# Kernel optimization log

Measured on AMD Instinct MI355X. Metric: run time of the kernel, lower is better.

Reference implementation:

```python
import jax, jax.numpy as jnp
import numpy as np

N = 10000        # nodes
E = 320000       # edges (avg degree 32)
W = 256          # width (assert width >= 256)
H = 8            # num_head (RESCALE_EDGE assumed (1,1) -> nhead=8, dhead=32)
D = W // H       # per-head dim
BOND = 33        # EMBED_BOND[0]
BAG = 3          # indices per edge bag
EPS_GN = 1e-5


def setup_inputs() -> dict:
    key = jax.random.key(0)
    ks = jax.random.split(key, 12)
    x = jax.random.normal(ks[0], (N, W), dtype=jnp.float32)
    edge_idx = jax.random.randint(ks[1], (2, E), 0, N)
    edge_attr = jax.random.randint(ks[2], (E, BAG), 0, BOND)
    # node in-degree wrt scatter target edge_idx[1], clamped to >= 1
    deg = jax.ops.segment_sum(jnp.ones((E,), jnp.float32), edge_idx[1], num_segments=N)
    deg = jnp.maximum(deg, 1.0)
    s = 1.0 / np.sqrt(W)
    W_src = jax.random.normal(ks[3], (W, W), dtype=jnp.float32) * s
    W_tgt = jax.random.normal(ks[4], (W, W), dtype=jnp.float32) * s
    emb = jax.random.normal(ks[5], (BOND, W), dtype=jnp.float32) * 0.02
    emb = emb.at[0].set(0.0)  # padding_idx=0 row is zeros
    sd = 1.0 / np.sqrt(D)
    W_gate = jax.random.normal(ks[6], (H, D, D), dtype=jnp.float32) * sd  # grouped conv1d k=1
    W_val = jax.random.normal(ks[7], (H, D, D), dtype=jnp.float32) * sd
    W_post = jax.random.normal(ks[8], (W, W), dtype=jnp.float32) * s
    deg_param = jnp.zeros((W,), jnp.float32) - 0.01  # DegreeLayer degree_init
    return {"x": x, "deg": deg, "edge_idx": edge_idx, "edge_attr": edge_attr,
            "W_src": W_src, "W_tgt": W_tgt, "emb": emb,
            "W_gate": W_gate, "W_val": W_val, "W_post": W_post,
            "deg_param": deg_param}


def reference(x, deg, edge_idx, edge_attr, W_src, W_tgt, emb, W_gate, W_val, W_post, deg_param):
    # src/tgt 1x1 Conv1d == per-node linear, then edge gather
    xs = x @ W_src.T                      # [N, W]
    xt = x @ W_tgt.T                      # [N, W]
    xx = xs[edge_idx[0]] + xt[edge_idx[1]]  # [E, W]

    # EmbeddingBag(mode='mean', padding_idx=0): padded entries excluded
    mask = (edge_attr != 0).astype(xx.dtype)            # [E, BAG]
    bag = jnp.einsum('ebc,eb->ec', emb[edge_attr], mask)  # [E, W]
    cnt = jnp.maximum(mask.sum(-1, keepdims=True), 1.0)
    gate_bias = bag / cnt

    # GroupNorm(H, W, affine=False) over [E, W, 1]
    xg = xx.reshape(-1, H, D)
    mu = xg.mean(-1, keepdims=True)
    var = xg.var(-1, keepdims=True)
    xn = (xg - mu) / jnp.sqrt(var + EPS_GN)              # [E, H, D]

    # gated grouped 1x1 convs (dropout is identity at eval)
    gin = xn + gate_bias.reshape(-1, H, D)
    gate = jax.nn.relu(jnp.einsum('ehd,hfd->ehf', gin, W_gate))
    val = jnp.einsum('ehd,hfd->ehf', xn, W_val)
    act = (gate * val).reshape(-1, W)                    # [E, W]
    out_e = act @ W_post.T                               # [E, W]

    # scatter-sum to nodes, then degree rescale
    agg = jax.ops.segment_sum(out_e, edge_idx[1], num_segments=x.shape[0])
    return jnp.power(deg[:, None], deg_param) * agg      # [N, W]
```

## Files before the change

### kernel.cpp

```cpp
#include <hip/hip_runtime.h>

#define WID 256
#define EPS_GN 1e-5f

typedef __bf16 v8bf __attribute__((ext_vector_type(8)));
typedef float  v4f  __attribute__((ext_vector_type(4)));

__device__ inline unsigned short f2b(float f) {
    unsigned int u = __builtin_bit_cast(unsigned int, f);
    unsigned int r = (u + 0x7fffu + ((u >> 16) & 1u)) >> 16;
    return (unsigned short)r;
}
__device__ inline __bf16 f2bf(float f) {
    unsigned short s = f2b(f);
    return __builtin_bit_cast(__bf16, s);
}
__device__ inline float lo16(unsigned int u) { return __builtin_bit_cast(float, u << 16); }
__device__ inline float hi16(unsigned int u) { return __builtin_bit_cast(float, u & 0xffff0000u); }

__device__ inline v8bf ld_w8(const float* __restrict__ p) {
    float4 a = *(const float4*)p, b = *(const float4*)(p + 4);
    v8bf r;
    r[0] = f2bf(a.x); r[1] = f2bf(a.y); r[2] = f2bf(a.z); r[3] = f2bf(a.w);
    r[4] = f2bf(b.x); r[5] = f2bf(b.y); r[6] = f2bf(b.z); r[7] = f2bf(b.w);
    return r;
}

__global__ __launch_bounds__(256, 2)
void prepproj_k(const float* __restrict__ x, const float* __restrict__ Wsrc,
                const float* __restrict__ Wtgt, const float* __restrict__ Wp,
                const float* __restrict__ Wg, const float* __restrict__ Wv,
                const float* __restrict__ emb, const int* __restrict__ eidx,
                unsigned short* __restrict__ xsb, unsigned short* __restrict__ xtb,
                unsigned short* __restrict__ Wpb, unsigned short* __restrict__ Wgb,
                unsigned short* __restrict__ Wvb, unsigned short* __restrict__ embWgT,
                int* __restrict__ cnt, float* __restrict__ aggact,
                int N, int E, int BOND, int PB, int AUX) {
    __shared__ unsigned short ab[32 * 264];
    int t = threadIdx.x, b = blockIdx.x;

    if (b >= PB) {
        int atid = (b - PB) * 256 + t, asz = AUX * 256;
        for (int i = atid; i < 65536; i += asz) Wpb[i] = f2b(Wp[i]);
        for (int i = atid; i < 8192; i += asz) { Wgb[i] = f2b(Wg[i]); Wvb[i] = f2b(Wv[i]); }
        for (int i = atid; i < 16384; i += asz) {
            int j = i >> 6, k = i & 63;
            float sacc = 0.f;
            if (k < BOND) {
                int h = j >> 5, f = j & 31;
                const float* er = emb + (size_t)k * WID + h * 32;
                const float* wr = Wg + h * 1024 + f * 32;
#pragma unroll
                for (int d = 0; d < 32; d++) sacc += er[d] * wr[d];
            }
            embWgT[j * 64 + k] = f2b(sacc);
        }
        {
            float4* ap = (float4*)aggact;
            int n4 = (N * WID) >> 2;
            for (int i = atid; i < n4; i += asz) ap[i] = make_float4(0.f, 0.f, 0.f, 0.f);
        }
        for (int i = atid; i < E; i += asz) atomicAdd(&cnt[eidx[E + i]], 1);
        return;
    }

    int n0 = b * 32;
#pragma unroll
    for (int ch = 0; ch < 8; ch++) {
        int flat = ch * 1024 + t * 4;
        int row = flat >> 8, col = flat & 255;
        int n = n0 + row;
        float4 v = (n < N) ? *(const float4*)&x[(size_t)n * WID + col]
                           : make_float4(0.f, 0.f, 0.f, 0.f);
        unsigned int p0 = (unsigned int)f2b(v.x) | ((unsigned int)f2b(v.y) << 16);
        unsigned int p1 = (unsigned int)f2b(v.z) | ((unsigned int)f2b(v.w) << 16);
        *(uint2*)&ab[row * 264 + col] = make_uint2(p0, p1);
    }
    __syncthreads();
    int w = t >> 6, lane = t & 63, m = lane & 15, kg = lane >> 4;
#pragma unroll
    for (int pass = 0; pass < 2; pass++) {
        const float* Wf = pass ? Wtgt : Wsrc;
        unsigned short* outp = pass ? xtb : xsb;
        v4f acc[2][4];
#pragma unroll
        for (int mt = 0; mt < 2; mt++)
#pragma unroll
            for (int nt = 0; nt < 4; nt++) acc[mt][nt] = (v4f){0.f, 0.f, 0.f, 0.f};
#pragma unroll
        for (int kt = 0; kt < 8; kt++) {
            int k0 = kt * 32 + kg * 8;
            v8bf a0 = *(const v8bf*)&ab[m * 264 + k0];
            v8bf a1 = *(const v8bf*)&ab[(16 + m) * 264 + k0];
#pragma unroll
            for (int nt = 0; nt < 4; nt++) {
                int j = w * 64 + nt * 16 + m;
                v8bf bfr = ld_w8(&Wf[j * 256 + k0]);
                acc[0][nt] = __builtin_amdgcn_mfma_f32_16x16x32_bf16(a0, bfr, acc[0][nt], 0, 0, 0);
                acc[1][nt] = __builtin_amdgcn_mfma_f32_16x16x32_bf16(a1, bfr, acc[1][nt], 0, 0, 0);
            }
        }
#pragma unroll
        for (int mt = 0; mt < 2; mt++)
#pragma unroll
            for (int r = 0; r < 4; r++) {
                int n = n0 + mt * 16 + kg * 4 + r;
                if (n < N)
#pragma unroll
                    for (int nt = 0; nt < 4; nt++)
                        outp[(size_t)n * WID + w * 64 + nt * 16 + m] = f2b(acc[mt][nt][r]);
            }
    }
}

__global__ void scan_k(const int* __restrict__ cnt, int* __restrict__ cur, int N) {
    __shared__ int part[1024];
    int t = threadIdx.x;
    int C = (N + 1023) / 1024;
    int s = 0;
    for (int i = 0; i < C; i++) { int idx = t * C + i; if (idx < N) s += cnt[idx]; }
    part[t] = s;
    __syncthreads();
    for (int d = 1; d < 1024; d <<= 1) {
        int v = (t >= d) ? part[t - d] : 0;
        __syncthreads();
        part[t] += v;
        __syncthreads();
    }
    int base = (t == 0) ? 0 : part[t - 1];
    for (int i = 0; i < C; i++) {
        int idx = t * C + i;
        if (idx < N) { cur[idx] = base; base += cnt[idx]; }
    }
}

__global__ void scat_k(const int* __restrict__ eidx, int* __restrict__ cur,
                       int* __restrict__ perm, int E) {
    int i = blockIdx.x * 256 + threadIdx.x;
    if (i < E) { int p = atomicAdd(&cur[eidx[E + i]], 1); perm[p] = i; }
}

__global__ __launch_bounds__(256, 7)
void edge_k(const unsigned short* __restrict__ xsb, const unsigned short* __restrict__ xtb,
            const int* __restrict__ eidx, const int* __restrict__ eattr,
            const int* __restrict__ perm, const unsigned short* __restrict__ Wgb,
            const unsigned short* __restrict__ Wvb, const unsigned short* __restrict__ embWgT,
            float* __restrict__ aggact, int E) {
    __shared__ unsigned short xxb[8704];
    __shared__ unsigned short Mld[32 * 72];
    __shared__ int src_s[32], tgt_s[32];
    __shared__ int segmask_s;

    int t = threadIdx.x;
    int e0 = blockIdx.x * 32;
    int ne = min(32, E - e0);

    {
        int tgtv = -1;
        if (t < 32) {
            int p = (t < ne) ? perm[e0 + t] : -1;
            src_s[t] = (p >= 0) ? eidx[p] : 0;
            tgtv = (p >= 0) ? eidx[E + p] : -1;
            tgt_s[t] = (tgtv >= 0) ? tgtv : 0;
            int a0 = 0, a1 = 0, a2 = 0;
            if (p >= 0) {
                const int* ap = eattr + (size_t)p * 3;
                a0 = ap[0]; a1 = ap[1]; a2 = ap[2];
            }
            unsigned int* Mr = (unsigned int*)&Mld[t * 72];
#pragma unroll
            for (int q = 0; q < 32; q++) Mr[q] = 0;
            int c = (a0 != 0) + (a1 != 0) + (a2 != 0);
            float inv = (p >= 0 && c > 0) ? 1.f / (float)c : 0.f;
            float wa = inv * (float)(1 + (a1 == a0) + (a2 == a0));
            float wb = inv * (float)(1 + (a2 == a1));
            Mld[t * 72 + a0] = f2b(wa);
            if (a1 != a0) Mld[t * 72 + a1] = f2b(wb);
            if (a2 != a0 && a2 != a1) Mld[t * 72 + a2] = f2b(inv);
        }
        if (t < 64) {
            int nxt = __shfl_down(tgtv, 1);
            bool flag = (t < ne) && ((t == ne - 1) || (nxt != tgtv));
            unsigned long long bal = __ballot(flag);
            if (t == 0) segmask_s = (int)(unsigned int)bal;
        }
    }
    __syncthreads();

    {
        int e = t >> 3, c = t & 7;
        int sn = src_s[e], g = tgt_s[e];
        bool live = (e < ne);
        const uint4* ps = (const uint4*)(xsb + (size_t)sn * WID);
        const uint4* pt = (const uint4*)(xtb + (size_t)g * WID);
        uint4 us[4], ut[4];
#pragma unroll
        for (int i = 0; i < 4; i++) { us[i] = ps[c + 8 * i]; ut[i] = pt[c + 8 * i]; }
        float v[4][8], sum[4], sq[4];
#pragma unroll
        for (int i = 0; i < 4; i++) {
            const unsigned int* au = (const unsigned int*)&us[i];
            const unsigned int* bu = (const unsigned int*)&ut[i];
            sum[i] = 0.f; sq[i] = 0.f;
#pragma unroll
            for (int q = 0; q < 4; q++) {
                float x0 = lo16(au[q]) + lo16(bu[q]);
                float x1 = hi16(au[q]) + hi16(bu[q]);
                if (!live) { x0 = 0.f; x1 = 0.f; }
                v[i][2 * q] = x0; v[i][2 * q + 1] = x1;
                sum[i] += x0 + x1;
                sq[i] += x0 * x0 + x1 * x1;
            }
        }
#pragma unroll
        for (int mask = 1; mask <= 2; mask <<= 1)
#pragma unroll
            for (int i = 0; i < 4; i++) {
                sum[i] += __shfl_xor(sum[i], mask);
                sq[i]  += __shfl_xor(sq[i], mask);
            }
#pragma unroll
        for (int i = 0; i < 4; i++) {
            float mu = sum[i] * (1.f / 32.f);
            float var = sq[i] * (1.f / 32.f) - mu * mu;
            float rs = rsqrtf(var + EPS_GN);
            unsigned int pk[4];
#pragma unroll
            for (int q = 0; q < 4; q++) {
                unsigned int l = f2b((v[i][2 * q] - mu) * rs);
                unsigned int h = f2b((v[i][2 * q + 1] - mu) * rs);
                pk[q] = l | (h << 16);
            }
            *(uint4*)&xxb[e * 264 + (c + 8 * i) * 8] = make_uint4(pk[0], pk[1], pk[2], pk[3]);
        }
    }
    __syncthreads();

    {
        int w = t >> 6, lane = t & 63, m = lane & 15, kg = lane >> 4;
        v8bf axn[2][2], aM[2][2];
#pragma unroll
        for (int mt = 0; mt < 2; mt++) {
            int row = mt * 16 + m;
            axn[0][mt] = *(const v8bf*)&xxb[row * 264 + (w * 2 + 0) * 32 + kg * 8];
            axn[1][mt] = *(const v8bf*)&xxb[row * 264 + (w * 2 + 1) * 32 + kg * 8];
            aM[mt][0] = *(const v8bf*)&Mld[row * 72 + kg * 8];
            aM[mt][1] = *(const v8bf*)&Mld[row * 72 + 32 + kg * 8];
        }
        __syncthreads();
        v4f z = {0.f, 0.f, 0.f, 0.f};
#pragma unroll
        for (int hh = 0; hh < 2; hh++) {
            int h = w * 2 + hh;
#pragma unroll
            for (int nt = 0; nt < 2; nt++) {
                int fj = nt * 16 + m;
                int j = h * 32 + fj;
                v8bf bWg = *(const v8bf*)&Wgb[h * 1024 + fj * 32 + kg * 8];
                v8bf bWv = *(const v8bf*)&Wvb[h * 1024 + fj * 32 + kg * 8];
                v8bf bE0 = *(const v8bf*)&embWgT[j * 64 + kg * 8];
                v8bf bE1 = *(const v8bf*)&embWgT[j * 64 + 32 + kg * 8];
#pragma unroll
                for (int mt = 0; mt < 2; mt++) {
                    v4f cgm = __builtin_amdgcn_mfma_f32_16x16x32_bf16(axn[hh][mt], bWg, z, 0, 0, 0);
                    cgm = __builtin_amdgcn_mfma_f32_16x16x32_bf16(aM[mt][0], bE0, cgm, 0, 0, 0);
                    cgm = __builtin_amdgcn_mfma_f32_16x16x32_bf16(aM[mt][1], bE1, cgm, 0, 0, 0);
                    v4f cv = __builtin_amdgcn_mfma_f32_16x16x32_bf16(axn[hh][mt], bWv, z, 0, 0, 0);
#pragma unroll
                    for (int r = 0; r < 4; r++) {
                        int e = mt * 16 + kg * 4 + r;
                        xxb[j * 34 + e] = f2b(fmaxf(cgm[r], 0.f) * cv[r]);
                    }
                }
            }
        }
    }
    __syncthreads();

    {
        unsigned int mask = (unsigned int)__builtin_amdgcn_readfirstlane(segmask_s);
        float sum = 0.f;
#pragma unroll
        for (int i = 0; i < 16; i++) {
            unsigned int r = *(const unsigned int*)&xxb[t * 34 + 2 * i];
            sum += lo16(r);
            if ((mask >> (2 * i)) & 1) {
                int tg = __builtin_amdgcn_readfirstlane(tgt_s[2 * i]);
                atomicAdd(&aggact[(size_t)tg * WID + t], sum);
                sum = 0.f;
            }
            sum += hi16(r);
            if ((mask >> (2 * i + 1)) & 1) {
                int tg = __builtin_amdgcn_readfirstlane(tgt_s[2 * i + 1]);
                atomicAdd(&aggact[(size_t)tg * WID + t], sum);
                sum = 0.f;
            }
        }
    }
}

__global__ __launch_bounds__(256, 2)
void post_k(const float* __restrict__ aggact, const unsigned short* __restrict__ Wpb,
            const float* __restrict__ deg, const float* __restrict__ dp,
            float* __restrict__ out, int N) {
    __shared__ unsigned short ab[32 * 264];
    __shared__ float degl[32];
    int t = threadIdx.x;
    int n0 = blockIdx.x * 32;
#pragma unroll
    for (int ch = 0; ch < 8; ch++) {
        int flat = ch * 1024 + t * 4;
        int row = flat >> 8, col = flat & 255;
        int n = n0 + row;
        float4 v = (n < N) ? *(const float4*)&aggact[(size_t)n * WID + col]
                           : make_float4(0.f, 0.f, 0.f, 0.f);
        unsigned int p0 = (unsigned int)f2b(v.x) | ((unsigned int)f2b(v.y) << 16);
        unsigned int p1 = (unsigned int)f2b(v.z) | ((unsigned int)f2b(v.w) << 16);
        *(uint2*)&ab[row * 264 + col] = make_uint2(p0, p1);
    }
    if (t < 32) {
        int n = n0 + t;
        degl[t] = (n < N) ? log2f(deg[n]) : 0.f;
    }
    __syncthreads();
    int w = t >> 6, lane = t & 63, m = lane & 15, kg = lane >> 4;
    v4f acc[2][4];
#pragma unroll
    for (int mt = 0; mt < 2; mt++)
#pragma unroll
        for (int nt = 0; nt < 4; nt++) acc[mt][nt] = (v4f){0.f, 0.f, 0.f, 0.f};
#pragma unroll
    for (int kt = 0; kt < 8; kt++) {
        int k0 = kt * 32 + kg * 8;
        v8bf a0 = *(const v8bf*)&ab[m * 264 + k0];
        v8bf a1 = *(const v8bf*)&ab[(16 + m) * 264 + k0];
#pragma unroll
        for (int nt = 0; nt < 4; nt++) {
            int j = w * 64 + nt * 16 + m;
            v8bf b = *(const v8bf*)&Wpb[j * 256 + k0];
            acc[0][nt] = __builtin_amdgcn_mfma_f32_16x16x32_bf16(a0, b, acc[0][nt], 0, 0, 0);
            acc[1][nt] = __builtin_amdgcn_mfma_f32_16x16x32_bf16(a1, b, acc[1][nt], 0, 0, 0);
        }
    }
    float dpv[4];
#pragma unroll
    for (int nt = 0; nt < 4; nt++) dpv[nt] = dp[w * 64 + nt * 16 + m];
#pragma unroll
    for (int mt = 0; mt < 2; mt++)
#pragma unroll
        for (int r = 0; r < 4; r++) {
            int row = mt * 16 + kg * 4 + r;
            int n = n0 + row;
            if (n < N) {
                float ld = degl[row];
#pragma unroll
                for (int nt = 0; nt < 4; nt++)
                    out[(size_t)n * WID + w * 64 + nt * 16 + m] =
                        exp2f(dpv[nt] * ld) * acc[mt][nt][r];
            }
        }
}

extern "C" void kernel_launch(void* const* d_in, const int* in_sizes, int n_in,
                              void* d_out, int out_size, void* d_ws, size_t ws_size,
                              hipStream_t stream) {
    const float* x    = (const float*)d_in[0];
    const float* deg  = (const float*)d_in[1];
    const int*   eidx = (const int*)d_in[2];
    const int*   eatt = (const int*)d_in[3];
    const float* Wsrc = (const float*)d_in[4];
    const float* Wtgt = (const float*)d_in[5];
    const float* emb  = (const float*)d_in[6];
    const float* Wg   = (const float*)d_in[7];
    const float* Wv   = (const float*)d_in[8];
    const float* Wp   = (const float*)d_in[9];
    const float* dp   = (const float*)d_in[10];
    int N = in_sizes[0] / WID;
    int E = in_sizes[2] / 2;
    int BOND = in_sizes[6] / WID;

    float* ws     = (float*)d_ws;
    float* aggact = ws;
    int*   cnt    = (int*)(aggact + (size_t)N * WID);
    int*   cur    = cnt + N;
    int*   perm   = cur + N;
    unsigned short* xsb = (unsigned short*)(perm + E);
    unsigned short* xtb = xsb + (size_t)N * WID;
    unsigned short* Wpb = xtb + (size_t)N * WID;
    unsigned short* Wgb = Wpb + 65536;
    unsigned short* Wvb = Wgb + 8192;
    unsigned short* embWgT = Wvb + 8192;

    int PB = (N + 31) / 32;
    int AUX = 128;

    hipMemsetAsync(cnt, 0, (size_t)N * sizeof(int), stream);
    prepproj_k<<<PB + AUX, 256, 0, stream>>>(x, Wsrc, Wtgt, Wp, Wg, Wv, emb, eidx,
                                             xsb, xtb, Wpb, Wgb, Wvb, embWgT, cnt, aggact,
                                             N, E, BOND, PB, AUX);
    scan_k<<<1, 1024, 0, stream>>>(cnt, cur, N);
    scat_k<<<(E + 255) / 256, 256, 0, stream>>>(eidx, cur, perm, E);
    edge_k<<<(E + 31) / 32, 256, 0, stream>>>(xsb, xtb, eidx, eatt, perm, Wgb, Wvb, embWgT, aggact, E);
    post_k<<<(N + 31) / 32, 256, 0, stream>>>(aggact, Wpb, deg, dp, (float*)d_out, N);
}
```

Measured before the change: 237.4 us.

## Use packed bf16 conversion, fdot2 pair sums, and XCD-aware edge tile mapping

Replaces the scalar round-to-nearest bf16 conversions with the hardware packed cvt_pk_bf16_f32 builtin where it is available. It folds the GroupNorm normalize into a single fma and packs the gated activations as 32-bit LDS stores. It also uses fdot2 with a ones vector to add bf16 pairs in the segmented reduction. Finally, it remaps edge block indices so that each of the 8 XCDs gets a contiguous range of sorted edge tiles, which should improve L2 locality for the atomics on target rows, though the grid may now contain a few idle blocks.

```diff
diff --git a/kernel.cpp b/kernel.cpp
--- a/kernel.cpp
+++ b/kernel.cpp
@@ -4,6 +4,7 @@
 #define EPS_GN 1e-5f
 
 typedef __bf16 v8bf __attribute__((ext_vector_type(8)));
+typedef __bf16 v2bf __attribute__((ext_vector_type(2)));
 typedef float  v4f  __attribute__((ext_vector_type(4)));
 
 __device__ inline unsigned short f2b(float f) {
@@ -18,12 +19,35 @@
 __device__ inline float lo16(unsigned int u) { return __builtin_bit_cast(float, u << 16); }
 __device__ inline float hi16(unsigned int u) { return __builtin_bit_cast(float, u & 0xffff0000u); }
 
+#if __has_builtin(__builtin_amdgcn_cvt_pk_bf16_f32)
+__device__ inline unsigned int pkbf(float a, float b) {
+    v2bf r = __builtin_amdgcn_cvt_pk_bf16_f32(a, b);
+    return __builtin_bit_cast(unsigned int, r);
+}
+#else
+__device__ inline unsigned int pkbf(float a, float b) {
+    return (unsigned int)f2b(a) | ((unsigned int)f2b(b) << 16);
+}
+#endif
+
+#if __has_builtin(__builtin_amdgcn_fdot2_f32_bf16)
+__device__ inline float pairsum(unsigned int u, float s) {
+    v2bf p = __builtin_bit_cast(v2bf, u);
+    v2bf ones = __builtin_bit_cast(v2bf, 0x3f803f80u);
+    return __builtin_amdgcn_fdot2_f32_bf16(p, ones, s, false);
+}
+#else
+__device__ inline float pairsum(unsigned int u, float s) {
+    return s + lo16(u) + hi16(u);
+}
+#endif
+
 __device__ inline v8bf ld_w8(const float* __restrict__ p) {
     float4 a = *(const float4*)p, b = *(const float4*)(p + 4);
-    v8bf r;
-    r[0] = f2bf(a.x); r[1] = f2bf(a.y); r[2] = f2bf(a.z); r[3] = f2bf(a.w);
-    r[4] = f2bf(b.x); r[5] = f2bf(b.y); r[6] = f2bf(b.z); r[7] = f2bf(b.w);
-    return r;
+    unsigned int u0 = pkbf(a.x, a.y), u1 = pkbf(a.z, a.w);
+    unsigned int u2 = pkbf(b.x, b.y), u3 = pkbf(b.z, b.w);
+    uint4 pk = make_uint4(u0, u1, u2, u3);
+    return __builtin_bit_cast(v8bf, pk);
 }
 
 __global__ __launch_bounds__(256, 2)
@@ -72,9 +96,7 @@
         int n = n0 + row;
         float4 v = (n < N) ? *(const float4*)&x[(size_t)n * WID + col]
                            : make_float4(0.f, 0.f, 0.f, 0.f);
-        unsigned int p0 = (unsigned int)f2b(v.x) | ((unsigned int)f2b(v.y) << 16);
-        unsigned int p1 = (unsigned int)f2b(v.z) | ((unsigned int)f2b(v.w) << 16);
-        *(uint2*)&ab[row * 264 + col] = make_uint2(p0, p1);
+        *(uint2*)&ab[row * 264 + col] = make_uint2(pkbf(v.x, v.y), pkbf(v.z, v.w));
     }
     __syncthreads();
     int w = t >> 6, lane = t & 63, m = lane & 15, kg = lane >> 4;
@@ -145,14 +167,16 @@
             const int* __restrict__ eidx, const int* __restrict__ eattr,
             const int* __restrict__ perm, const unsigned short* __restrict__ Wgb,
             const unsigned short* __restrict__ Wvb, const unsigned short* __restrict__ embWgT,
-            float* __restrict__ aggact, int E) {
+            float* __restrict__ aggact, int E, int NT, int PER) {
     __shared__ unsigned short xxb[8704];
     __shared__ unsigned short Mld[32 * 72];
     __shared__ int src_s[32], tgt_s[32];
     __shared__ int segmask_s;
 
+    int tile = (blockIdx.x & 7) * PER + (blockIdx.x >> 3);
+    if (tile >= NT) return;
     int t = threadIdx.x;
-    int e0 = blockIdx.x * 32;
+    int e0 = tile * 32;
     int ne = min(32, E - e0);
 
     {
@@ -224,13 +248,11 @@
             float mu = sum[i] * (1.f / 32.f);
             float var = sq[i] * (1.f / 32.f) - mu * mu;
             float rs = rsqrtf(var + EPS_GN);
+            float nmr = -mu * rs;
             unsigned int pk[4];
 #pragma unroll
-            for (int q = 0; q < 4; q++) {
-                unsigned int l = f2b((v[i][2 * q] - mu) * rs);
-                unsigned int h = f2b((v[i][2 * q + 1] - mu) * rs);
-                pk[q] = l | (h << 16);
-            }
+            for (int q = 0; q < 4; q++)
+                pk[q] = pkbf(fmaf(v[i][2 * q], rs, nmr), fmaf(v[i][2 * q + 1], rs, nmr));
             *(uint4*)&xxb[e * 264 + (c + 8 * i) * 8] = make_uint4(pk[0], pk[1], pk[2], pk[3]);
         }
     }
@@ -266,11 +288,13 @@
                     cgm = __builtin_amdgcn_mfma_f32_16x16x32_bf16(aM[mt][0], bE0, cgm, 0, 0, 0);
                     cgm = __builtin_amdgcn_mfma_f32_16x16x32_bf16(aM[mt][1], bE1, cgm, 0, 0, 0);
                     v4f cv = __builtin_amdgcn_mfma_f32_16x16x32_bf16(axn[hh][mt], bWv, z, 0, 0, 0);
-#pragma unroll
-                    for (int r = 0; r < 4; r++) {
-                        int e = mt * 16 + kg * 4 + r;
-                        xxb[j * 34 + e] = f2b(fmaxf(cgm[r], 0.f) * cv[r]);
-                    }
+                    float a0 = fmaxf(cgm[0], 0.f) * cv[0];
+                    float a1 = fmaxf(cgm[1], 0.f) * cv[1];
+                    float a2 = fmaxf(cgm[2], 0.f) * cv[2];
+                    float a3 = fmaxf(cgm[3], 0.f) * cv[3];
+                    int e0i = mt * 16 + kg * 4;
+                    *(unsigned int*)&xxb[j * 34 + e0i]     = pkbf(a0, a1);
+                    *(unsigned int*)&xxb[j * 34 + e0i + 2] = pkbf(a2, a3);
                 }
             }
         }
@@ -283,17 +307,23 @@
 #pragma unroll
         for (int i = 0; i < 16; i++) {
             unsigned int r = *(const unsigned int*)&xxb[t * 34 + 2 * i];
-            sum += lo16(r);
-            if ((mask >> (2 * i)) & 1) {
+            if (!((mask >> (2 * i)) & 1)) {
+                sum = pairsum(r, sum);
+                if ((mask >> (2 * i + 1)) & 1) {
+                    int tg = __builtin_amdgcn_readfirstlane(tgt_s[2 * i + 1]);
+                    atomicAdd(&aggact[(size_t)tg * WID + t], sum);
+                    sum = 0.f;
+                }
+            } else {
+                sum += lo16(r);
                 int tg = __builtin_amdgcn_readfirstlane(tgt_s[2 * i]);
                 atomicAdd(&aggact[(size_t)tg * WID + t], sum);
-                sum = 0.f;
-            }
-            sum += hi16(r);
-            if ((mask >> (2 * i + 1)) & 1) {
-                int tg = __builtin_amdgcn_readfirstlane(tgt_s[2 * i + 1]);
-                atomicAdd(&aggact[(size_t)tg * WID + t], sum);
-                sum = 0.f;
+                sum = hi16(r);
+                if ((mask >> (2 * i + 1)) & 1) {
+                    int tg2 = __builtin_amdgcn_readfirstlane(tgt_s[2 * i + 1]);
+                    atomicAdd(&aggact[(size_t)tg2 * WID + t], sum);
+                    sum = 0.f;
+                }
             }
         }
     }
@@ -314,9 +344,7 @@
         int n = n0 + row;
         float4 v = (n < N) ? *(const float4*)&aggact[(size_t)n * WID + col]
                            : make_float4(0.f, 0.f, 0.f, 0.f);
-        unsigned int p0 = (unsigned int)f2b(v.x) | ((unsigned int)f2b(v.y) << 16);
-        unsigned int p1 = (unsigned int)f2b(v.z) | ((unsigned int)f2b(v.w) << 16);
-        *(uint2*)&ab[row * 264 + col] = make_uint2(p0, p1);
+        *(uint2*)&ab[row * 264 + col] = make_uint2(pkbf(v.x, v.y), pkbf(v.z, v.w));
     }
     if (t < 32) {
         int n = n0 + t;
@@ -393,6 +421,8 @@
 
     int PB = (N + 31) / 32;
     int AUX = 128;
+    int NT = (E + 31) / 32;
+    int PER = (NT + 7) / 8;
 
     hipMemsetAsync(cnt, 0, (size_t)N * sizeof(int), stream);
     prepproj_k<<<PB + AUX, 256, 0, stream>>>(x, Wsrc, Wtgt, Wp, Wg, Wv, emb, eidx,
@@ -400,6 +430,7 @@
                                              N, E, BOND, PB, AUX);
     scan_k<<<1, 1024, 0, stream>>>(cnt, cur, N);
     scat_k<<<(E + 255) / 256, 256, 0, stream>>>(eidx, cur, perm, E);
-    edge_k<<<(E + 31) / 32, 256, 0, stream>>>(xsb, xtb, eidx, eatt, perm, Wgb, Wvb, embWgT, aggact, E);
+    edge_k<<<PER * 8, 256, 0, stream>>>(xsb, xtb, eidx, eatt, perm, Wgb, Wvb, embWgT,
+                                        aggact, E, NT, PER);
     post_k<<<(N + 31) / 32, 256, 0, stream>>>(aggact, Wpb, deg, dp, (float*)d_out, N);
 }
```

After: 235.9 us. No clear change (-0.6%).
